# Kernel optimization log

Hardware: AMD Instinct MI355X
Metric: run time of the kernel (lower is better)

Reference implementation:

```python
import jax, jax.numpy as jnp
import numpy as np

HIDDEN = 2048
HEADS = 16
HEAD_DIM = HIDDEN // HEADS
GS = 0.1          # governance_strength
ROPE_BASE = 10000.0


def _rope_tables(seq_len, dtype=jnp.float32):
    inv_freq = 1.0 / (ROPE_BASE ** (jnp.arange(0, HEAD_DIM, 2, dtype=jnp.float32) / HEAD_DIM))
    t = jnp.arange(seq_len, dtype=jnp.float32)
    freqs = jnp.outer(t, inv_freq)                      # [S, head_dim/2]
    return jnp.cos(freqs).astype(dtype), jnp.sin(freqs).astype(dtype)


def _apply_rope(x, cos, sin):
    # x: [B, S, H, Dh]; cos/sin: [S, Dh/2] -> broadcast over batch and heads
    c = cos[None, :, None, :]
    s = sin[None, :, None, :]
    x1, x2 = jnp.split(x, 2, axis=-1)
    return jnp.concatenate([x1 * c - x2 * s, x2 * c + x1 * s], axis=-1)


def setup_inputs() -> dict:
    key = jax.random.key(0)
    ks = jax.random.split(key, 9)
    B, S = 2, 1024
    x = jax.random.normal(ks[0], (B, S, HIDDEN), dtype=jnp.float32)
    prophetic_mask = jax.random.normal(ks[1], (B, HEADS, S, S), dtype=jnp.float32)
    policy_mask = jax.random.normal(ks[2], (B, HEADS, S, S), dtype=jnp.float32)
    memory_weights = jax.random.uniform(ks[3], (B, HEADS, S, S), dtype=jnp.float32)
    sd = 1.0 / np.sqrt(HIDDEN)
    Wq = jax.random.normal(ks[4], (HIDDEN, HIDDEN), dtype=jnp.float32) * sd
    Wk = jax.random.normal(ks[5], (HIDDEN, HIDDEN), dtype=jnp.float32) * sd
    Wv = jax.random.normal(ks[6], (HIDDEN, HIDDEN), dtype=jnp.float32) * sd
    Wo = jax.random.normal(ks[7], (HIDDEN, HIDDEN), dtype=jnp.float32) * sd
    bo = jax.random.normal(ks[8], (HIDDEN,), dtype=jnp.float32) * 0.01
    return {"x": x, "prophetic_mask": prophetic_mask, "policy_mask": policy_mask,
            "memory_weights": memory_weights, "Wq": Wq, "Wk": Wk, "Wv": Wv,
            "Wo": Wo, "bo": bo}


def reference(x, prophetic_mask, policy_mask, memory_weights, Wq, Wk, Wv, Wo, bo):
    B, S, D = x.shape
    scale = HEAD_DIM ** -0.5
    # QKV projections (bias=False)
    q = (x @ Wq).reshape(B, S, HEADS, HEAD_DIM)
    k = (x @ Wk).reshape(B, S, HEADS, HEAD_DIM)
    v = (x @ Wv).reshape(B, S, HEADS, HEAD_DIM)
    cos, sin = _rope_tables(S, x.dtype)
    q = _apply_rope(q, cos, sin)
    k = _apply_rope(k, cos, sin)
    # [B, H, S, Dh]
    q = q.transpose(0, 2, 1, 3)
    k = k.transpose(0, 2, 1, 3)
    v = v.transpose(0, 2, 1, 3)
    scores = jnp.einsum('bhqd,bhkd->bhqk', q, k) * scale
    # Combined governance bias: prophetic*gs*0.5 + policy*gs + log(1 + mem*gs + 1e-8)
    bias = (prophetic_mask * (GS * 0.5)
            + policy_mask * GS
            + jnp.log(1.0 + memory_weights * GS + 1e-8))
    scores = scores + bias
    causal = jnp.tril(jnp.ones((S, S), dtype=bool))  # [S, S]
    scores = jnp.where(causal[None, None], scores, -jnp.inf)
    attn = jax.nn.softmax(scores, axis=-1)
    out = jnp.einsum('bhqk,bhkd->bhqd', attn, v)
    out = out.transpose(0, 2, 1, 3).reshape(B, S, D)
    return out @ Wo + bo
```

## Files before the change

### kernel.cpp

```cpp
#include <hip/hip_runtime.h>

typedef unsigned int u32;
typedef unsigned short u16;
typedef __bf16 bf16x8 __attribute__((ext_vector_type(8)));
typedef float f32x4 __attribute__((ext_vector_type(4)));

#define HIDDEN 2048
#define HEADS 16
#define HDIM 128
#define SEQ 1024
#define BATCH 2
#define ROWS (BATCH*SEQ)
#define SCALE 0.08838834764831845f
#define GSC 0.1f

__device__ __forceinline__ u16 f2bf(float f) {
    u32 x = __builtin_bit_cast(u32, f);
    x += 0x7fffu + ((x >> 16) & 1u);
    return (u16)(x >> 16);
}
__device__ __forceinline__ float bf2f(u16 u) {
    return __builtin_bit_cast(float, ((u32)u) << 16);
}
__device__ __forceinline__ void gld_lds16(const void* g, void* l) {
    __builtin_amdgcn_global_load_lds((const __attribute__((address_space(1))) u32*)g,
                                     (__attribute__((address_space(3))) u32*)l, 16, 0, 0);
}

__global__ __launch_bounds__(256) void k_prep(
    const float* __restrict__ x, u16* __restrict__ xb,
    const float* __restrict__ W0, const float* __restrict__ W1,
    const float* __restrict__ W2, const float* __restrict__ W3,
    u16* __restrict__ T0, u16* __restrict__ T1, u16* __restrict__ T2, u16* __restrict__ T3,
    float* __restrict__ cosT, float* __restrict__ sinT) {
    __shared__ float t[32][33];
    const int bid = blockIdx.x;
    const int tid = threadIdx.x;
    if (bid < 4096) {
        const int i = (bid * 256 + tid) * 4;
        float4 v = *(const float4*)(x + i);
        uint2 r;
        r.x = (u32)f2bf(v.x) | ((u32)f2bf(v.y) << 16);
        r.y = (u32)f2bf(v.z) | ((u32)f2bf(v.w) << 16);
        *(uint2*)(xb + i) = r;
    } else if (bid < 4096 + 16384) {
        const int idx = bid - 4096;
        const int bx = (idx & 63) * 32, by = ((idx >> 6) & 63) * 32, z = idx >> 12;
        const float* W = (z == 0) ? W0 : (z == 1) ? W1 : (z == 2) ? W2 : W3;
        u16* Wt = (z == 0) ? T0 : (z == 1) ? T1 : (z == 2) ? T2 : T3;
        const int tx = tid & 31, ty = tid >> 5;
#pragma unroll
        for (int yy = 0; yy < 32; yy += 8)
            t[ty + yy][tx] = W[(size_t)(by + ty + yy) * HIDDEN + bx + tx];
        __syncthreads();
#pragma unroll
        for (int yy = 0; yy < 32; yy += 8)
            Wt[(size_t)(bx + ty + yy) * HIDDEN + by + tx] = f2bf(t[tx][ty + yy]);
    } else {
        const int i = (bid - 20480) * 256 + tid;
        const int s = i >> 6, d = i & 63;
        const float inv = expf(-(float)d * 0.14391156831f);
        const float fr = (float)s * inv;
        cosT[i] = cosf(fr);
        sinT[i] = sinf(fr);
    }
}

__global__ __launch_bounds__(512, 2) void k_qkv(
    const u16* __restrict__ Ag, const u16* __restrict__ Bg,
    u16* __restrict__ qo, u16* __restrict__ ko, u16* __restrict__ vo) {
    __shared__ __align__(16) u16 As[2][16384];
    __shared__ __align__(16) u16 Bs[2][16384];
    const int tid = threadIdx.x;
    const int l = tid & 63, wid = tid >> 6;
    const int wr = wid >> 2, wc = wid & 3;
    const int g = l >> 4, l15 = l & 15;
    const int bid = blockIdx.x;
    const int idx = bid >> 3;
    const int nt = (bid & 7) * 3 + idx % 3;
    const int mt = idx / 3;
    const int m0 = mt * 256, n0 = nt * 256;
    const int swxe = (l15 & 7) << 3;
    int srow[4], scol[4];
#pragma unroll
    for (int p = 0; p < 4; ++p) {
        const int o = p * 8192 + tid * 16;
        const int r = o >> 7;
        srow[p] = r;
        scol[p] = ((o & 127) ^ ((r & 7) << 4)) >> 1;
    }
    f32x4 acc[8][4] = {};
    constexpr int NT = HIDDEN / 64;

#pragma unroll
    for (int p = 0; p < 4; ++p)
        gld_lds16(Ag + (size_t)(m0 + srow[p]) * HIDDEN + scol[p], &As[0][p * 4096 + tid * 8]);
#pragma unroll
    for (int p = 0; p < 4; ++p)
        gld_lds16(Bg + (size_t)(n0 + srow[p]) * HIDDEN + scol[p], &Bs[0][p * 4096 + tid * 8]);

    for (int i = 0; i < NT; ++i) {
        const int cur = i & 1, nb = cur ^ 1;
        const bool more = (i + 1 < NT);
        if (more) {
            const int kk1 = (i + 1) * 64;
#pragma unroll
            for (int p = 0; p < 4; ++p)
                gld_lds16(Ag + (size_t)(m0 + srow[p]) * HIDDEN + kk1 + scol[p],
                          &As[nb][p * 4096 + tid * 8]);
#pragma unroll
            for (int p = 0; p < 4; ++p)
                gld_lds16(Bg + (size_t)(n0 + srow[p]) * HIDDEN + kk1 + scol[p],
                          &Bs[nb][p * 4096 + tid * 8]);
        }
        if (more) asm volatile("s_waitcnt vmcnt(8)" ::: "memory");
        else      asm volatile("s_waitcnt vmcnt(0)" ::: "memory");
        __builtin_amdgcn_sched_barrier(0);
        __builtin_amdgcn_s_barrier();
        bf16x8 bfr[4][2];
#pragma unroll
        for (int n = 0; n < 4; ++n)
#pragma unroll
            for (int ks = 0; ks < 2; ++ks)
                bfr[n][ks] = *(const bf16x8*)&Bs[cur][(wc * 64 + n * 16 + l15) * 64 +
                                                      ((ks * 32 + g * 8) ^ swxe)];
        __builtin_amdgcn_s_setprio(1);
#pragma unroll
        for (int m = 0; m < 8; ++m) {
            bf16x8 a0 = *(const bf16x8*)&As[cur][(wr * 128 + m * 16 + l15) * 64 +
                                                 ((g * 8) ^ swxe)];
            bf16x8 a1 = *(const bf16x8*)&As[cur][(wr * 128 + m * 16 + l15) * 64 +
                                                 ((32 + g * 8) ^ swxe)];
#pragma unroll
            for (int n = 0; n < 4; ++n) {
                acc[m][n] = __builtin_amdgcn_mfma_f32_16x16x32_bf16(a0, bfr[n][0], acc[m][n], 0, 0, 0);
                acc[m][n] = __builtin_amdgcn_mfma_f32_16x16x32_bf16(a1, bfr[n][1], acc[m][n], 0, 0, 0);
            }
        }
        __builtin_amdgcn_s_setprio(0);
        asm volatile("s_waitcnt lgkmcnt(0)" ::: "memory");
        __builtin_amdgcn_sched_barrier(0);
        __builtin_amdgcn_s_barrier();
    }
    u16* Cb = (nt < 8) ? qo : (nt < 16) ? ko : vo;
    const int nloc = n0 & 2047;
#pragma unroll
    for (int m = 0; m < 8; ++m)
#pragma unroll
        for (int n = 0; n < 4; ++n) {
            const int col = nloc + wc * 64 + n * 16 + l15;
#pragma unroll
            for (int j = 0; j < 4; ++j) {
                const int row = m0 + wr * 128 + m * 16 + g * 4 + j;
                Cb[(size_t)row * HIDDEN + col] = f2bf(acc[m][n][j]);
            }
        }
}

__global__ __launch_bounds__(256) void k_mid(
    u16* __restrict__ q, u16* __restrict__ k,
    const float* __restrict__ cosT, const float* __restrict__ sinT,
    const u16* __restrict__ v, u16* __restrict__ vT) {
    __shared__ u16 t[32][33];
    const int bid = blockIdx.x;
    const int tid = threadIdx.x;
    if (bid < 8192) {
        const int i = bid * 256 + tid;
        const int row = i >> 10;
        const int hd = i & 1023;
        const int h = hd >> 6, d = hd & 63;
        const int s = row & (SEQ - 1);
        const float c = cosT[s * 64 + d], sn = sinT[s * 64 + d];
        const size_t o1 = (size_t)row * HIDDEN + h * HDIM + d;
        const size_t o2 = o1 + 64;
        float x1 = bf2f(q[o1]), x2 = bf2f(q[o2]);
        q[o1] = f2bf(x1 * c - x2 * sn);
        q[o2] = f2bf(x2 * c + x1 * sn);
        float y1 = bf2f(k[o1]), y2 = bf2f(k[o2]);
        k[o1] = f2bf(y1 * c - y2 * sn);
        k[o2] = f2bf(y2 * c + y1 * sn);
    } else {
        const int idx = bid - 8192;
        const int s0 = (idx & 31) * 32, d0 = ((idx >> 5) & 3) * 32, bh = idx >> 7;
        const int b = bh >> 4, h = bh & 15;
        const int tx = tid & 31, ty = tid >> 5;
#pragma unroll
        for (int yy = 0; yy < 32; yy += 8)
            t[ty + yy][tx] = v[(size_t)(b * SEQ + s0 + ty + yy) * HIDDEN + h * HDIM + d0 + tx];
        __syncthreads();
#pragma unroll
        for (int yy = 0; yy < 32; yy += 8)
            vT[((size_t)bh * HDIM + d0 + ty + yy) * SEQ + s0 + tx] = t[tx][ty + yy];
    }
}

__global__ __launch_bounds__(128) void k_attn(
    const u16* __restrict__ qraw, const u16* __restrict__ kraw, const u16* __restrict__ vT,
    const float* __restrict__ pm, const float* __restrict__ po, const float* __restrict__ mw,
    u16* __restrict__ attnb) {
    __shared__ __align__(16) u16 Ks[64 * 128];
    __shared__ __align__(16) u16 Vs[128 * 64];
    __shared__ __align__(16) u16 Pl[2][16 * 72];
    const int tid = threadIdx.x;
    const int ln = tid & 63, w = tid >> 6;
    const int g = ln >> 4, q15 = ln & 15;
    const int j = blockIdx.x;
    const int p = j >> 3;
    const int y = (j & 7) * 4 + (p & 3);
    const int t = p >> 2;
    const int hi = t >> 3, lo = t & 7;
    const int qb = hi * 8 + ((hi & 1) ? 7 - lo : lo);
    const int b = y >> 4, h = y & 15;
    const int q0 = qb * 32;
    const int qw = q0 + w * 16;
    const int qg = qw + q15;
    const int ktmax = qb >> 1;
    const int k_r = tid >> 4;
    const int k_c = ((tid & 15) * 8) ^ ((k_r & 7) << 3);
    const int v_r = tid >> 3;
    const int v_c = ((tid & 7) * 8) ^ ((v_r & 7) << 3);
    const int sw = (q15 & 7) << 3;
    bf16x8 qf[4];
    {
        const size_t qoff = (size_t)(b * SEQ + qg) * HIDDEN + h * HDIM;
#pragma unroll
        for (int ds = 0; ds < 4; ++ds) qf[ds] = *(const bf16x8*)(qraw + qoff + ds * 32 + g * 8);
    }
    f32x4 acc_o[8] = {};
    float m_run = -1e30f, l_run = 0.f;
    u16* pw = &Pl[w][0];
    const u16* krow = kraw + (size_t)(b * SEQ) * HIDDEN + h * HDIM;
    const u16* vrow = vT + (size_t)y * HDIM * SEQ;
    const size_t mbase = ((size_t)y * SEQ + qg) * SEQ + g * 4;
    const float* pmr = pm + mbase;
    const float* por = po + mbase;
    const float* mwr = mw + mbase;

    float4 mA[12], mB[12];
    auto issue_masks = [&](float4 (&mm)[12], int kt) {
        const int c = kt * 64;
#pragma unroll
        for (int m = 0; m < 4; ++m) {
            mm[m * 3 + 0] = *(const float4*)(pmr + c + m * 16);
            mm[m * 3 + 1] = *(const float4*)(por + c + m * 16);
            mm[m * 3 + 2] = *(const float4*)(mwr + c + m * 16);
        }
    };

    auto step = [&](int kt, float4 (&cur)[12], float4 (&nxt)[12]) {
        const int k0 = kt * 64;
#pragma unroll
        for (int c = 0; c < 8; ++c)
            gld_lds16(krow + (size_t)(k0 + c * 8 + k_r) * HIDDEN + k_c, &Ks[c * 1024 + tid * 8]);
#pragma unroll
        for (int c = 0; c < 8; ++c)
            gld_lds16(vrow + (size_t)(c * 16 + v_r) * SEQ + k0 + v_c, &Vs[c * 1024 + tid * 8]);
        __syncthreads();
        f32x4 accs[4] = {};
#pragma unroll
        for (int ds = 0; ds < 4; ++ds)
#pragma unroll
            for (int m = 0; m < 4; ++m) {
                bf16x8 kf = *(const bf16x8*)&Ks[(m * 16 + q15) * 128 + ((ds * 32 + g * 8) ^ sw)];
                accs[m] = __builtin_amdgcn_mfma_f32_16x16x32_bf16(kf, qf[ds], accs[m], 0, 0, 0);
            }
        if (kt < ktmax) issue_masks(nxt, kt + 1);
        float pmax = -1e30f;
#pragma unroll
        for (int m = 0; m < 4; ++m) {
            const float4 av = cur[m * 3 + 0];
            const float4 bv4 = cur[m * 3 + 1];
            const float4 cv = cur[m * 3 + 2];
#pragma unroll
            for (int r = 0; r < 4; ++r) {
                const int kglob = k0 + m * 16 + g * 4 + r;
                const float bias = (&av.x)[r] * (GSC * 0.5f) + (&bv4.x)[r] * GSC +
                                   __logf(fmaf((&cv.x)[r], GSC, 1.0f + 1e-8f));
                float s = (kglob <= qg) ? fmaf(accs[m][r], SCALE, bias) : -1e30f;
                accs[m][r] = s;
                pmax = fmaxf(pmax, s);
            }
        }
        pmax = fmaxf(pmax, __shfl_xor(pmax, 16));
        pmax = fmaxf(pmax, __shfl_xor(pmax, 32));
        const float mnew = fmaxf(m_run, pmax);
        const float alpha = __expf(m_run - mnew);
        float lsum = 0.f;
#pragma unroll
        for (int m = 0; m < 4; ++m)
#pragma unroll
            for (int r = 0; r < 4; ++r) {
                float e = __expf(accs[m][r] - mnew);
                accs[m][r] = e;
                lsum += e;
            }
        lsum += __shfl_xor(lsum, 16);
        lsum += __shfl_xor(lsum, 32);
        l_run = l_run * alpha + lsum;
        m_run = mnew;
#pragma unroll
        for (int m = 0; m < 4; ++m) {
            uint2 pk;
            pk.x = (u32)f2bf(accs[m][0]) | ((u32)f2bf(accs[m][1]) << 16);
            pk.y = (u32)f2bf(accs[m][2]) | ((u32)f2bf(accs[m][3]) << 16);
            *(uint2*)&pw[q15 * 72 + m * 16 + g * 4] = pk;
        }
        float al[4];
#pragma unroll
        for (int jj = 0; jj < 4; ++jj) al[jj] = __shfl(alpha, g * 4 + jj);
#pragma unroll
        for (int n = 0; n < 8; ++n)
#pragma unroll
            for (int jj = 0; jj < 4; ++jj) acc_o[n][jj] *= al[jj];
#pragma unroll
        for (int c = 0; c < 2; ++c) {
            const bf16x8 af = *(const bf16x8*)&pw[q15 * 72 + c * 32 + g * 8];
#pragma unroll
            for (int n = 0; n < 8; ++n) {
                const bf16x8 vf = *(const bf16x8*)&Vs[(n * 16 + q15) * 64 + ((c * 32 + g * 8) ^ sw)];
                acc_o[n] = __builtin_amdgcn_mfma_f32_16x16x32_bf16(af, vf, acc_o[n], 0, 0, 0);
            }
        }
        __syncthreads();
    };

    issue_masks(mA, 0);
    int kt = 0;
    for (;;) {
        step(kt, mA, mB);
        if (kt == ktmax) break;
        ++kt;
        step(kt, mB, mA);
        if (kt == ktmax) break;
        ++kt;
    }

    const float linv = 1.0f / l_run;
    float li[4];
#pragma unroll
    for (int jj = 0; jj < 4; ++jj) li[jj] = __shfl(linv, g * 4 + jj);
#pragma unroll
    for (int n = 0; n < 8; ++n)
#pragma unroll
        for (int jj = 0; jj < 4; ++jj) {
            const int row = b * SEQ + qw + g * 4 + jj;
            const int col = h * HDIM + n * 16 + q15;
            attnb[(size_t)row * HIDDEN + col] = f2bf(acc_o[n][jj] * li[jj]);
        }
}

__global__ __launch_bounds__(256) void k_out(
    const u16* __restrict__ A, const u16* __restrict__ Bt,
    float* __restrict__ Cf, const float* __restrict__ bias) {
    __shared__ __align__(16) u16 As[2][8192];
    __shared__ __align__(16) u16 Bs[2][8192];
    const int tid = threadIdx.x;
    const int l = tid & 63, wid = tid >> 6;
    const int wr = wid >> 1, wc = wid & 1;
    const int g = l >> 4, l15 = l & 15;
    const int bid = blockIdx.x;
    const int rr = (bid & 7) * 32 + (bid >> 3);
    const int mt = rr >> 4, nt = rr & 15;
    const int m0 = mt * 128, n0 = nt * 128;
    const int swxe = (l15 & 7) << 3;
    int srow[4], scol[4];
#pragma unroll
    for (int p = 0; p < 4; ++p) {
        const int o = p * 4096 + tid * 16;
        const int r = o >> 7;
        srow[p] = r;
        scol[p] = ((o & 127) ^ ((r & 7) << 4)) >> 1;
    }
    f32x4 acc[4][4] = {};
    constexpr int NT = HIDDEN / 64;

#pragma unroll
    for (int p = 0; p < 4; ++p) {
        gld_lds16(A + (size_t)(m0 + srow[p]) * HIDDEN + scol[p], &As[0][p * 2048 + tid * 8]);
        gld_lds16(Bt + (size_t)(n0 + srow[p]) * HIDDEN + scol[p], &Bs[0][p * 2048 + tid * 8]);
    }

    for (int i = 0; i < NT; ++i) {
        const int cur = i & 1, nb = cur ^ 1;
        const bool more = (i + 1 < NT);
        if (more) {
            const int kk1 = (i + 1) * 64;
#pragma unroll
            for (int p = 0; p < 4; ++p) {
                gld_lds16(A + (size_t)(m0 + srow[p]) * HIDDEN + kk1 + scol[p],
                          &As[nb][p * 2048 + tid * 8]);
                gld_lds16(Bt + (size_t)(n0 + srow[p]) * HIDDEN + kk1 + scol[p],
                          &Bs[nb][p * 2048 + tid * 8]);
            }
        }
        if (more) asm volatile("s_waitcnt vmcnt(8)" ::: "memory");
        else      asm volatile("s_waitcnt vmcnt(0)" ::: "memory");
        __builtin_amdgcn_sched_barrier(0);
        __builtin_amdgcn_s_barrier();
        bf16x8 bfr[4][2];
#pragma unroll
        for (int n = 0; n < 4; ++n)
#pragma unroll
            for (int ks = 0; ks < 2; ++ks)
                bfr[n][ks] = *(const bf16x8*)&Bs[cur][(wc * 64 + n * 16 + l15) * 64 +
                                                      ((ks * 32 + g * 8) ^ swxe)];
        __builtin_amdgcn_s_setprio(1);
#pragma unroll
        for (int m = 0; m < 4; ++m) {
            bf16x8 a0 = *(const bf16x8*)&As[cur][(wr * 64 + m * 16 + l15) * 64 +
                                                 ((g * 8) ^ swxe)];
            bf16x8 a1 = *(const bf16x8*)&As[cur][(wr * 64 + m * 16 + l15) * 64 +
                                                 ((32 + g * 8) ^ swxe)];
#pragma unroll
            for (int n = 0; n < 4; ++n) {
                acc[m][n] = __builtin_amdgcn_mfma_f32_16x16x32_bf16(a0, bfr[n][0], acc[m][n], 0, 0, 0);
                acc[m][n] = __builtin_amdgcn_mfma_f32_16x16x32_bf16(a1, bfr[n][1], acc[m][n], 0, 0, 0);
            }
        }
        __builtin_amdgcn_s_setprio(0);
        asm volatile("s_waitcnt lgkmcnt(0)" ::: "memory");
        __builtin_amdgcn_sched_barrier(0);
        __builtin_amdgcn_s_barrier();
    }
#pragma unroll
    for (int m = 0; m < 4; ++m)
#pragma unroll
        for (int n = 0; n < 4; ++n) {
            const int col = n0 + wc * 64 + n * 16 + l15;
#pragma unroll
            for (int j = 0; j < 4; ++j) {
                const int row = m0 + wr * 64 + m * 16 + g * 4 + j;
                Cf[(size_t)row * HIDDEN + col] = acc[m][n][j] + bias[col];
            }
        }
}

extern "C" void kernel_launch(void* const* d_in, const int* in_sizes, int n_in,
                              void* d_out, int out_size, void* d_ws, size_t ws_size,
                              hipStream_t stream) {
    (void)in_sizes; (void)n_in; (void)out_size; (void)ws_size;
    const float* x  = (const float*)d_in[0];
    const float* pm = (const float*)d_in[1];
    const float* po = (const float*)d_in[2];
    const float* mw = (const float*)d_in[3];
    const float* Wq = (const float*)d_in[4];
    const float* Wk = (const float*)d_in[5];
    const float* Wv = (const float*)d_in[6];
    const float* Wo = (const float*)d_in[7];
    const float* bo = (const float*)d_in[8];
    float* out = (float*)d_out;

    char* ws = (char*)d_ws;
    const size_t SZ = (size_t)ROWS * HIDDEN;
    const size_t OFF = SZ * 2;
    u16* xb    = (u16*)(ws + 0 * OFF);
    u16* Wqt   = (u16*)(ws + 1 * OFF);
    u16* Wkt   = (u16*)(ws + 2 * OFF);
    u16* Wvt   = (u16*)(ws + 3 * OFF);
    u16* Wot   = (u16*)(ws + 4 * OFF);
    u16* qrawp = (u16*)(ws + 5 * OFF);
    u16* krawp = (u16*)(ws + 6 * OFF);
    u16* vrawp = (u16*)(ws + 7 * OFF);
    u16* vTp   = (u16*)(ws + 8 * OFF);
    u16* attnb = (u16*)(ws + 9 * OFF);
    float* cosT = (float*)(ws + 10 * OFF);
    float* sinT = (float*)(ws + 10 * OFF + 262144);

    k_prep<<<dim3(20736), 256, 0, stream>>>(x, xb, Wq, Wk, Wv, Wo,
                                            Wqt, Wkt, Wvt, Wot, cosT, sinT);
    k_qkv<<<dim3(192), 512, 0, stream>>>(xb, Wqt, qrawp, krawp, vrawp);
    k_mid<<<dim3(12288), 256, 0, stream>>>(qrawp, krawp, cosT, sinT, vrawp, vTp);
    k_attn<<<dim3(1024), 128, 0, stream>>>(qrawp, krawp, vTp, pm, po, mw, attnb);
    k_out<<<dim3(256), 256, 0, stream>>>(attnb, Wot, out, bo);
}
```

Measured before the change: 230.8 us.

## Double-buffer K/V tiles and enlarge attention blocks to 64 queries with four waves

```diff
diff --git a/kernel.cpp b/kernel.cpp
--- a/kernel.cpp
+++ b/kernel.cpp
@@ -194,13 +194,13 @@
     }
 }
 
-__global__ __launch_bounds__(128) void k_attn(
+__global__ __launch_bounds__(256) void k_attn(
     const u16* __restrict__ qraw, const u16* __restrict__ kraw, const u16* __restrict__ vT,
     const float* __restrict__ pm, const float* __restrict__ po, const float* __restrict__ mw,
     u16* __restrict__ attnb) {
-    __shared__ __align__(16) u16 Ks[64 * 128];
-    __shared__ __align__(16) u16 Vs[128 * 64];
-    __shared__ __align__(16) u16 Pl[2][16 * 72];
+    __shared__ __align__(16) u16 Ks[2][64 * 128];
+    __shared__ __align__(16) u16 Vs[2][128 * 64];
+    __shared__ __align__(16) u16 Pl[4][16 * 72];
     const int tid = threadIdx.x;
     const int ln = tid & 63, w = tid >> 6;
     const int g = ln >> 4, q15 = ln & 15;
@@ -208,13 +208,12 @@
     const int p = j >> 3;
     const int y = (j & 7) * 4 + (p & 3);
     const int t = p >> 2;
-    const int hi = t >> 3, lo = t & 7;
-    const int qb = hi * 8 + ((hi & 1) ? 7 - lo : lo);
+    const int qb = (t < 8) ? (15 - 2 * t) : (2 * (t - 8));
     const int b = y >> 4, h = y & 15;
-    const int q0 = qb * 32;
+    const int q0 = qb * 64;
     const int qw = q0 + w * 16;
     const int qg = qw + q15;
-    const int ktmax = qb >> 1;
+    const int ktmax = qb;
     const int k_r = tid >> 4;
     const int k_c = ((tid & 15) * 8) ^ ((k_r & 7) << 3);
     const int v_r = tid >> 3;
@@ -236,6 +235,17 @@
     const float* por = po + mbase;
     const float* mwr = mw + mbase;
 
+    auto stage_kv = [&](int kt, int bufi) {
+        const int k0 = kt * 64;
+#pragma unroll
+        for (int c = 0; c < 4; ++c)
+            gld_lds16(krow + (size_t)(k0 + c * 16 + k_r) * HIDDEN + k_c,
+                      &Ks[bufi][c * 2048 + tid * 8]);
+#pragma unroll
+        for (int c = 0; c < 4; ++c)
+            gld_lds16(vrow + (size_t)(c * 32 + v_r) * SEQ + k0 + v_c,
+                      &Vs[bufi][c * 2048 + tid * 8]);
+    };
     float4 mA[12], mB[12];
     auto issue_masks = [&](float4 (&mm)[12], int kt) {
         const int c = kt * 64;
@@ -248,23 +258,26 @@
     };
 
     auto step = [&](int kt, float4 (&cur)[12], float4 (&nxt)[12]) {
+        const int bufi = kt & 1;
+        const bool more = (kt < ktmax);
+        if (more) {
+            stage_kv(kt + 1, bufi ^ 1);
+            issue_masks(nxt, kt + 1);
+        }
+        if (more) asm volatile("s_waitcnt vmcnt(20)" ::: "memory");
+        else      asm volatile("s_waitcnt vmcnt(0)" ::: "memory");
+        __builtin_amdgcn_sched_barrier(0);
+        __builtin_amdgcn_s_barrier();
         const int k0 = kt * 64;
-#pragma unroll
-        for (int c = 0; c < 8; ++c)
-            gld_lds16(krow + (size_t)(k0 + c * 8 + k_r) * HIDDEN + k_c, &Ks[c * 1024 + tid * 8]);
-#pragma unroll
-        for (int c = 0; c < 8; ++c)
-            gld_lds16(vrow + (size_t)(c * 16 + v_r) * SEQ + k0 + v_c, &Vs[c * 1024 + tid * 8]);
-        __syncthreads();
         f32x4 accs[4] = {};
 #pragma unroll
         for (int ds = 0; ds < 4; ++ds)
 #pragma unroll
             for (int m = 0; m < 4; ++m) {
-                bf16x8 kf = *(const bf16x8*)&Ks[(m * 16 + q15) * 128 + ((ds * 32 + g * 8) ^ sw)];
+                bf16x8 kf = *(const bf16x8*)&Ks[bufi][(m * 16 + q15) * 128 +
+                                                      ((ds * 32 + g * 8) ^ sw)];
                 accs[m] = __builtin_amdgcn_mfma_f32_16x16x32_bf16(kf, qf[ds], accs[m], 0, 0, 0);
             }
-        if (kt < ktmax) issue_masks(nxt, kt + 1);
         float pmax = -1e30f;
 #pragma unroll
         for (int m = 0; m < 4; ++m) {
@@ -317,13 +330,17 @@
             const bf16x8 af = *(const bf16x8*)&pw[q15 * 72 + c * 32 + g * 8];
 #pragma unroll
             for (int n = 0; n < 8; ++n) {
-                const bf16x8 vf = *(const bf16x8*)&Vs[(n * 16 + q15) * 64 + ((c * 32 + g * 8) ^ sw)];
+                const bf16x8 vf = *(const bf16x8*)&Vs[bufi][(n * 16 + q15) * 64 +
+                                                           ((c * 32 + g * 8) ^ sw)];
                 acc_o[n] = __builtin_amdgcn_mfma_f32_16x16x32_bf16(af, vf, acc_o[n], 0, 0, 0);
             }
         }
-        __syncthreads();
+        asm volatile("s_waitcnt lgkmcnt(0)" ::: "memory");
+        __builtin_amdgcn_sched_barrier(0);
+        __builtin_amdgcn_s_barrier();
     };
 
+    stage_kv(0, 0);
     issue_masks(mA, 0);
     int kt = 0;
     for (;;) {
@@ -470,6 +487,6 @@
                                             Wqt, Wkt, Wvt, Wot, cosT, sinT);
     k_qkv<<<dim3(192), 512, 0, stream>>>(xb, Wqt, qrawp, krawp, vrawp);
     k_mid<<<dim3(12288), 256, 0, stream>>>(qrawp, krawp, cosT, sinT, vrawp, vTp);
-    k_attn<<<dim3(1024), 128, 0, stream>>>(qrawp, krawp, vTp, pm, po, mw, attnb);
+    k_attn<<<dim3(512), 256, 0, stream>>>(qrawp, krawp, vTp, pm, po, mw, attnb);
     k_out<<<dim3(256), 256, 0, stream>>>(attnb, Wot, out, bo);
 }
```

New measurement: 265.0 us. 1.15x slower.
